# Kernel tuning notes

Measured on AMD Instinct MI355X. Metric: run time of the kernel, lower is better.

The kernel has to match this reference:

```python
import jax, jax.numpy as jnp
import numpy as np

B, S, C, H, D = 4, 1024, 1024, 16, 64
MAX_POS = 512
SPAN = min(max(S, S), MAX_POS)  # rel_attn_span = 512
SCALE = 1.0 / np.sqrt(3.0 * D)


def setup_inputs() -> dict:
    key = jax.random.key(0)
    ks = jax.random.split(key, 10)
    std = 0.02
    return {
        "hidden_states": jax.random.normal(ks[0], (B, S, C), jnp.float32),
        "rel_embeddings": jax.random.normal(ks[1], (2 * MAX_POS, C), jnp.float32),
        "Wq": jax.random.normal(ks[2], (C, H, D), jnp.float32) * std,
        "bq": jnp.zeros((H, D), jnp.float32),
        "Wk": jax.random.normal(ks[3], (C, H, D), jnp.float32) * std,
        "Wv": jax.random.normal(ks[4], (C, H, D), jnp.float32) * std,
        "bv": jnp.zeros((H, D), jnp.float32),
        "Wc2p": jax.random.normal(ks[5], (C, H, D), jnp.float32) * std,
        "Wp2c": jax.random.normal(ks[6], (C, H, D), jnp.float32) * std,
        "bp2c": jnp.zeros((H, D), jnp.float32),
        "Wo": jax.random.normal(ks[7], (C, C), jnp.float32) * std,
        "bo": jnp.zeros((C,), jnp.float32),
    }


def reference(hidden_states, rel_embeddings, Wq, bq, Wk, Wv, bv, Wc2p, Wp2c, bp2c, Wo, bo):
    # Projections: 'abc,cde->abde'  -> [B,S,H,D]
    q = jnp.einsum("bsc,chd->bshd", hidden_states, Wq) + bq
    k = jnp.einsum("bsc,chd->bshd", hidden_states, Wk)
    v = jnp.einsum("bsc,chd->bshd", hidden_states, Wv) + bv

    q = q * SCALE
    # content-to-content scores: 'aecd,abcd->acbe' -> [B,H,Q,K]
    scores = jnp.einsum("bkhd,bqhd->bhqk", k, q)

    # relative-position ids: rel_pos[q,k] = q - k, shape [S,S]
    ids = jnp.arange(S, dtype=jnp.int32)
    rel_pos = ids[:, None] - ids[None, :]

    # slice rel table to the active span (full table here since S >= MAX_POS)
    rel = rel_embeddings[MAX_POS - SPAN : MAX_POS + SPAN, :]  # [2*SPAN, C]

    # c2p: pos_key [2*SPAN,H,D]; scores [B,H,Q,2*SPAN]; gather along last axis
    pos_key = jnp.einsum("rc,chd->rhd", rel, Wc2p)
    c2p = jnp.einsum("bqhd,rhd->bhqr", q, pos_key)
    c2p_pos = jnp.clip(rel_pos + SPAN, 0, 2 * SPAN - 1)  # [Q,K]
    c2p_idx = jnp.broadcast_to(c2p_pos[None, None], (B, H, S, S))
    c2p_g = jnp.take_along_axis(c2p, c2p_idx, axis=-1)

    # p2c: pos_query (scaled) [2*SPAN,H,D]; scores [B,H,K,2*SPAN]
    pos_query = (jnp.einsum("rc,chd->rhd", rel, Wp2c) + bp2c) * SCALE
    p2c = jnp.einsum("bkhd,rhd->bhkr", k, pos_query)
    p2c_pos = jnp.clip(-rel_pos + SPAN, 0, 2 * SPAN - 1)  # [K,K]
    p2c_idx = jnp.broadcast_to(p2c_pos[None, None], (B, H, S, S))
    p2c_g = jnp.take_along_axis(p2c, p2c_idx, axis=-1)

    scores = scores + c2p_g + p2c_g
    # NOTE: source calls _masked_softmax without passing attention_mask -> plain softmax
    probs = jax.nn.softmax(scores, axis=-1)

    # 'acbe,aecd->abcd' -> [B,Q,H,D]
    attn_out = jnp.einsum("bhqk,bkhd->bqhd", probs, v)
    attn_out = attn_out.reshape(B, S, H * D)
    return jnp.einsum("bsc,cd->bsd", attn_out, Wo) + bo
```

## Files before the change

### kernel.cpp

```cpp
#include <hip/hip_runtime.h>
#include <cmath>

#define SCALE_F 0.07216878364870322f

typedef unsigned short u16;
typedef __attribute__((ext_vector_type(8))) __bf16 bf16x8;
typedef __attribute__((ext_vector_type(4))) float f32x4;
typedef __attribute__((ext_vector_type(16))) float f32x16;

#define MFMA16(a, b, c) __builtin_amdgcn_mfma_f32_16x16x32_bf16(a, b, c, 0, 0, 0)
#define MFMA32(a, b, c) __builtin_amdgcn_mfma_f32_32x32x16_bf16(a, b, c, 0, 0, 0)

__device__ __forceinline__ u16 f2bf(float x) {
    unsigned u = __float_as_uint(x);
    unsigned r = (u + 0x7fffu + ((u >> 16) & 1u)) >> 16;
    return (u16)r;
}
__device__ __forceinline__ float bf2f(u16 u) {
    return __uint_as_float(((unsigned)u) << 16);
}
__device__ __forceinline__ void split2(float x, u16& h, u16& l) {
    h = f2bf(x);
    l = f2bf(x - bf2f(h));
}

__device__ __forceinline__ void glds16(const u16* g, u16* s) {
    __builtin_amdgcn_global_load_lds(
        (const __attribute__((address_space(1))) unsigned int*)g,
        (__attribute__((address_space(3))) unsigned int*)s,
        16, 0, 0);
}

__device__ __forceinline__ bf16x8 frg(const u16* base, int row, int ch) {
    return *(const bf16x8*)(base + (row << 6) + ((ch ^ (row & 7)) << 3));
}

__global__ __launch_bounds__(256) void split_rows2(
    const float* __restrict__ x0, u16* __restrict__ h0, u16* __restrict__ l0,
    int nblk0,
    const float* __restrict__ x1, u16* __restrict__ h1, u16* __restrict__ l1)
{
    const float* x; u16* h; u16* l; int bx = blockIdx.x;
    if (bx < nblk0) { x = x0; h = h0; l = l0; }
    else { x = x1; h = h1; l = l1; bx -= nblk0; }
    int i = (bx * 256 + threadIdx.x) << 2;
    float4 v = *(const float4*)(x + i);
    ushort4 hv, lv;
    split2(v.x, hv.x, lv.x); split2(v.y, hv.y, lv.y);
    split2(v.z, hv.z, lv.z); split2(v.w, hv.w, lv.w);
    *(ushort4*)(h + i) = hv;
    *(ushort4*)(l + i) = lv;
}

__global__ __launch_bounds__(256) void transpose3(
    const float* __restrict__ W0, u16* __restrict__ Th0, u16* __restrict__ Tl0,
    const float* __restrict__ W1, u16* __restrict__ Th1, u16* __restrict__ Tl1,
    const float* __restrict__ W2, u16* __restrict__ Th2, u16* __restrict__ Tl2)
{
    const float* W; u16* Th; u16* Tl;
    if (blockIdx.z == 0)      { W = W0; Th = Th0; Tl = Tl0; }
    else if (blockIdx.z == 1) { W = W1; Th = Th1; Tl = Tl1; }
    else                      { W = W2; Th = Th2; Tl = Tl2; }
    __shared__ float t[64][65];
    const int tid = threadIdx.x;
    const int r = tid >> 4, c4 = (tid & 15) << 2;
    const int k0 = blockIdx.y << 6, n0 = blockIdx.x << 6;
#pragma unroll
    for (int p = 0; p < 4; ++p) {
        int row = (p << 4) + r;
        float4 v = *(const float4*)(W + (size_t)(k0 + row) * 1024 + n0 + c4);
        t[row][c4] = v.x; t[row][c4 + 1] = v.y; t[row][c4 + 2] = v.z; t[row][c4 + 3] = v.w;
    }
    __syncthreads();
#pragma unroll
    for (int p = 0; p < 4; ++p) {
        int nr = (p << 4) + r;
        float a = t[c4 + 0][nr];
        float b = t[c4 + 1][nr];
        float c = t[c4 + 2][nr];
        float d = t[c4 + 3][nr];
        ushort4 hv, lv;
        split2(a, hv.x, lv.x); split2(b, hv.y, lv.y);
        split2(c, hv.z, lv.z); split2(d, hv.w, lv.w);
        *(ushort4*)(Th + (size_t)(n0 + nr) * 1024 + k0 + c4) = hv;
        *(ushort4*)(Tl + (size_t)(n0 + nr) * 1024 + k0 + c4) = lv;
    }
}

struct GD {
    const u16 *Ah, *Al, *Bh, *Bl;
    const float* bias;
    float* Cf;
    u16 *Ch, *Cl;
    int N, K;
    float scale;
    int mode;
};

__global__ __launch_bounds__(256, 2) void gemm_mfma(GD d0, GD d1, int xsplit)
{
    __shared__ u16 sAh[128 * 32];
    __shared__ u16 sAl[128 * 32];
    __shared__ u16 sBh[128 * 32];
    __shared__ u16 sBl[128 * 32];

    const GD d = (blockIdx.x < (unsigned)xsplit) ? d0 : d1;
    const int bx = (blockIdx.x < (unsigned)xsplit) ? blockIdx.x : blockIdx.x - xsplit;
    const int N = d.N, K = d.K;

    const int tid = threadIdx.x;
    const int wv = tid >> 6, lane = tid & 63;
    const int quad = lane >> 4, ln = lane & 15;
    const int wr = wv & 1, wc = wv >> 1;
    const int m0 = blockIdx.y << 7, n0 = bx << 7;

    const u16* gsrc = (wv == 0) ? d.Ah : (wv == 1) ? d.Al : (wv == 2) ? d.Bh : d.Bl;
    u16* sdst = (wv == 0) ? sAh : (wv == 1) ? sAl : (wv == 2) ? sBh : sBl;
    const int row0 = (wv < 2) ? m0 : n0;
    const u16* gbase = gsrc + (size_t)(row0 + (lane >> 2)) * K + ((lane & 3) << 3);

    f32x4 acc[4][4];
#pragma unroll
    for (int f = 0; f < 4; ++f)
#pragma unroll
        for (int g = 0; g < 4; ++g) acc[f][g] = (f32x4){0.f, 0.f, 0.f, 0.f};

    const u16* pa_h = sAh + ((wr << 6) + ln) * 32 + (quad << 3);
    const u16* pa_l = sAl + ((wr << 6) + ln) * 32 + (quad << 3);
    const u16* pb_h = sBh + ((wc << 6) + ln) * 32 + (quad << 3);
    const u16* pb_l = sBl + ((wc << 6) + ln) * 32 + (quad << 3);

#pragma unroll
    for (int t = 0; t < 8; ++t)
        glds16(gbase + (size_t)(t << 4) * K, sdst + t * 512);

    for (int kt = 0; kt < K; kt += 32) {
        __syncthreads();
        bf16x8 bhv[4], blv[4], ahv[4], alv[4];
#pragma unroll
        for (int g = 0; g < 4; ++g) {
            bhv[g] = *(const bf16x8*)(pb_h + g * 512);
            blv[g] = *(const bf16x8*)(pb_l + g * 512);
            ahv[g] = *(const bf16x8*)(pa_h + g * 512);
            alv[g] = *(const bf16x8*)(pa_l + g * 512);
        }
        __syncthreads();
        if (kt + 32 < K) {
#pragma unroll
            for (int t = 0; t < 8; ++t)
                glds16(gbase + (size_t)(t << 4) * K + (kt + 32), sdst + t * 512);
        }
#pragma unroll
        for (int f = 0; f < 4; ++f) {
#pragma unroll
            for (int g = 0; g < 4; ++g) {
                acc[f][g] = MFMA16(ahv[f], bhv[g], acc[f][g]);
                acc[f][g] = MFMA16(ahv[f], blv[g], acc[f][g]);
                acc[f][g] = MFMA16(alv[f], bhv[g], acc[f][g]);
            }
        }
    }

    if (d.mode == 0) {
#pragma unroll
        for (int f = 0; f < 4; ++f) {
            int row = m0 + (wr << 6) + (f << 4) + (quad << 2);
#pragma unroll
            for (int g = 0; g < 4; ++g) {
                int col = n0 + (wc << 6) + (g << 4) + ln;
                float bb = d.bias ? d.bias[col] : 0.f;
#pragma unroll
                for (int r = 0; r < 4; ++r)
                    d.Cf[(size_t)(row + r) * N + col] = (acc[f][g][r] + bb) * d.scale;
            }
        }
    } else if (d.mode == 1) {
#pragma unroll
        for (int f = 0; f < 4; ++f) {
            int row = m0 + (wr << 6) + (f << 4) + (quad << 2);
#pragma unroll
            for (int g = 0; g < 4; ++g) {
                int col = n0 + (wc << 6) + (g << 4) + ln;
                float bb = d.bias ? d.bias[col] : 0.f;
#pragma unroll
                for (int r = 0; r < 4; ++r) {
                    float v = (acc[f][g][r] + bb) * d.scale;
                    u16 hh, ll;
                    split2(v, hh, ll);
                    d.Ch[(size_t)(row + r) * N + col] = hh;
                    d.Cl[(size_t)(row + r) * N + col] = ll;
                }
            }
        }
    } else if (d.mode == 2) {
#pragma unroll
        for (int f = 0; f < 4; ++f) {
            int row = m0 + (wr << 6) + (f << 4) + (quad << 2);
#pragma unroll
            for (int g = 0; g < 4; ++g) {
                int col = n0 + (wc << 6) + (g << 4) + ln;
                size_t obase = (size_t)(col >> 10) * 1048576 + (col & 1023);
#pragma unroll
                for (int r = 0; r < 4; ++r) {
                    float v = acc[f][g][r] + (d.bias ? d.bias[row + r] : 0.f);
                    u16 hh, ll;
                    split2(v, hh, ll);
                    size_t idx = obase + (size_t)(row + r) * 1024;
                    d.Ch[idx] = hh;
                    d.Cl[idx] = ll;
                }
            }
        }
    } else {
#pragma unroll
        for (int f = 0; f < 4; ++f) {
            int row = m0 + (wr << 6) + (f << 4) + (quad << 2);
#pragma unroll
            for (int g = 0; g < 4; ++g) {
                int col = n0 + (wc << 6) + (g << 4) + ln;
                float bb = d.bias ? d.bias[col] : 0.f;
#pragma unroll
                for (int r = 0; r < 4; ++r)
                    d.Ch[(size_t)(row + r) * N + col] =
                        f2bf((acc[f][g][r] + bb) * d.scale);
            }
        }
    }
}

__global__ __launch_bounds__(256, 2) void gemm_mfma_64(GD d0, GD d1, int xsplit)
{
    __shared__ u16 sAh[64 * 32];
    __shared__ u16 sAl[64 * 32];
    __shared__ u16 sBh[128 * 32];
    __shared__ u16 sBl[128 * 32];

    const GD d = (blockIdx.x < (unsigned)xsplit) ? d0 : d1;
    const int bx = (blockIdx.x < (unsigned)xsplit) ? blockIdx.x : blockIdx.x - xsplit;
    const int N = d.N, K = d.K;

    const int tid = threadIdx.x;
    const int wv = tid >> 6, lane = tid & 63;
    const int quad = lane >> 4, ln = lane & 15;
    const int wr = wv & 1, wc = wv >> 1;
    const int m0 = blockIdx.y << 6, n0 = bx << 7;

    const u16* gsrc = (wv == 0) ? d.Ah : (wv == 1) ? d.Al : (wv == 2) ? d.Bh : d.Bl;
    u16* sdst = (wv == 0) ? sAh : (wv == 1) ? sAl : (wv == 2) ? sBh : sBl;
    const int row0 = (wv < 2) ? m0 : n0;
    const int nt = (wv < 2) ? 4 : 8;
    const u16* gbase = gsrc + (size_t)(row0 + (lane >> 2)) * K + ((lane & 3) << 3);

    f32x4 acc[2][4];
#pragma unroll
    for (int f = 0; f < 2; ++f)
#pragma unroll
        for (int g = 0; g < 4; ++g) acc[f][g] = (f32x4){0.f, 0.f, 0.f, 0.f};

    const u16* pa_h = sAh + ((wr << 5) + ln) * 32 + (quad << 3);
    const u16* pa_l = sAl + ((wr << 5) + ln) * 32 + (quad << 3);
    const u16* pb_h = sBh + ((wc << 6) + ln) * 32 + (quad << 3);
    const u16* pb_l = sBl + ((wc << 6) + ln) * 32 + (quad << 3);

#pragma unroll
    for (int t = 0; t < 8; ++t)
        if (t < nt) glds16(gbase + (size_t)(t << 4) * K, sdst + t * 512);

    for (int kt = 0; kt < K; kt += 32) {
        __syncthreads();
        bf16x8 bhv[4], blv[4], ahv[2], alv[2];
#pragma unroll
        for (int g = 0; g < 4; ++g) {
            bhv[g] = *(const bf16x8*)(pb_h + g * 512);
            blv[g] = *(const bf16x8*)(pb_l + g * 512);
        }
#pragma unroll
        for (int f = 0; f < 2; ++f) {
            ahv[f] = *(const bf16x8*)(pa_h + f * 512);
            alv[f] = *(const bf16x8*)(pa_l + f * 512);
        }
        __syncthreads();
        if (kt + 32 < K) {
#pragma unroll
            for (int t = 0; t < 8; ++t)
                if (t < nt)
                    glds16(gbase + (size_t)(t << 4) * K + (kt + 32), sdst + t * 512);
        }
#pragma unroll
        for (int f = 0; f < 2; ++f) {
#pragma unroll
            for (int g = 0; g < 4; ++g) {
                acc[f][g] = MFMA16(ahv[f], bhv[g], acc[f][g]);
                acc[f][g] = MFMA16(ahv[f], blv[g], acc[f][g]);
                acc[f][g] = MFMA16(alv[f], bhv[g], acc[f][g]);
            }
        }
    }

    if (d.mode == 0) {
#pragma unroll
        for (int f = 0; f < 2; ++f) {
            int row = m0 + (wr << 5) + (f << 4) + (quad << 2);
#pragma unroll
            for (int g = 0; g < 4; ++g) {
                int col = n0 + (wc << 6) + (g << 4) + ln;
                float bb = d.bias ? d.bias[col] : 0.f;
#pragma unroll
                for (int r = 0; r < 4; ++r)
                    d.Cf[(size_t)(row + r) * N + col] = (acc[f][g][r] + bb) * d.scale;
            }
        }
    } else if (d.mode == 2) {
#pragma unroll
        for (int f = 0; f < 2; ++f) {
            int row = m0 + (wr << 5) + (f << 4) + (quad << 2);
#pragma unroll
            for (int g = 0; g < 4; ++g) {
                int col = n0 + (wc << 6) + (g << 4) + ln;
                size_t obase = (size_t)(col >> 10) * 1048576 + (col & 1023);
#pragma unroll
                for (int r = 0; r < 4; ++r) {
                    float v = acc[f][g][r] + (d.bias ? d.bias[row + r] : 0.f);
                    u16 hh, ll;
                    split2(v, hh, ll);
                    size_t idx = obase + (size_t)(row + r) * 1024;
                    d.Ch[idx] = hh;
                    d.Cl[idx] = ll;
                }
            }
        }
    } else if (d.mode == 3) {
#pragma unroll
        for (int f = 0; f < 2; ++f) {
            int row = m0 + (wr << 5) + (f << 4) + (quad << 2);
#pragma unroll
            for (int g = 0; g < 4; ++g) {
                int col = n0 + (wc << 6) + (g << 4) + ln;
                float bb = d.bias ? d.bias[col] : 0.f;
#pragma unroll
                for (int r = 0; r < 4; ++r)
                    d.Ch[(size_t)(row + r) * N + col] =
                        f2bf((acc[f][g][r] + bb) * d.scale);
            }
        }
    } else {
#pragma unroll
        for (int f = 0; f < 2; ++f) {
            int row = m0 + (wr << 5) + (f << 4) + (quad << 2);
#pragma unroll
            for (int g = 0; g < 4; ++g) {
                int col = n0 + (wc << 6) + (g << 4) + ln;
                float bb = d.bias ? d.bias[col] : 0.f;
#pragma unroll
                for (int r = 0; r < 4; ++r) {
                    float v = (acc[f][g][r] + bb) * d.scale;
                    u16 hh, ll;
                    split2(v, hh, ll);
                    d.Ch[(size_t)(row + r) * N + col] = hh;
                    d.Cl[(size_t)(row + r) * N + col] = ll;
                }
            }
        }
    }
}

__global__ __launch_bounds__(256, 2) void attn_mfma(
    const u16* Qh_g, const u16* Ql_g,
    const u16* __restrict__ Kh_g, const u16* __restrict__ Kl_g,
    const u16* __restrict__ VTh_g, const u16* __restrict__ VTl_g,
    const u16* __restrict__ PKh_g, const u16* __restrict__ PQh_g,
    u16* outh, u16* outl)
{
    __shared__ __align__(16) unsigned char smem[67840];
    u16* Kh_s  = (u16*)smem;
    u16* Kl_s  = (u16*)(smem + 8192);
    u16* PKs   = (u16*)(smem + 16384);
    u16* VTh_s = (u16*)(smem + 16384);
    u16* VTl_s = (u16*)(smem + 24576);
    u16* PQs   = (u16*)(smem + 32768);
    u16* Ph    = (u16*)(smem + 49152);
    u16* Pl    = (u16*)(smem + 58368);
    float* Mbase = (float*)(smem + 49152);
    float* l_s = (float*)(smem + 67584);

    const int tid = threadIdx.x;
    const int wv = tid >> 6, lane = tid & 63;
    const int half = lane >> 5, lc = lane & 31;
    const int rw = wv & 1, cw = wv >> 1;
    const int b = blockIdx.z, h = blockIdx.y;
    const int q0 = blockIdx.x << 6, hd0 = h << 6;
    float* Mw = Mbase + wv * 1056;

    const int rloc = lane >> 3;
    const int k4e  = (((lane & 7) ^ rloc) << 3);

    bf16x8 qfh[4], qfl[4], kfh[4], kfl[4];
    const size_t arow = ((size_t)(b * 1024 + q0 + (rw << 5) + lc) << 10) + hd0 + (half << 3);
    {
#pragma unroll
        for (int c = 0; c < 4; ++c) {
            qfh[c] = *(const bf16x8*)(Qh_g + arow + (c << 4));
            qfl[c] = *(const bf16x8*)(Ql_g + arow + (c << 4));
            kfh[c] = *(const bf16x8*)(Kh_g + arow + (c << 4));
            kfl[c] = *(const bf16x8*)(Kl_g + arow + (c << 4));
        }
    }
    if (tid < 64) l_s[tid] = 0.f;

    f32x16 o;
    float l_part[16];
#pragma unroll
    for (int r = 0; r < 16; ++r) { o[r] = 0.f; l_part[r] = 0.f; }

    const int sbC = (rw - cw + 1) << 5;
    const int sbP = (cw - rw + 1) << 5;

    {
#pragma unroll
        for (int t = 0; t < 2; ++t) {
            int call = wv + (t << 2);
            int row = (call << 3) + rloc;
            size_t g = ((size_t)(b * 1024 + 0 + row) << 10) + hd0 + k4e;
            glds16(Kh_g + g, Kh_s + (call << 9));
            glds16(Kl_g + g, Kl_s + (call << 9));
        }
        const int baseC = q0 + 449, baseP = -q0 + 449;
#pragma unroll
        for (int t = 0; t < 4; ++t) {
            int call = wv + (t << 2);
            int row = (call << 3) + rloc;
            int rc = min(max(baseC + row, 0), 1023);
            int rp = min(max(baseP + row, 0), 1023);
            glds16(PKh_g + (((size_t)rc << 10) + hd0 + k4e), PKs + (call << 9));
            glds16(PQh_g + (((size_t)rp << 10) + hd0 + k4e), PQs + (call << 9));
        }
    }
    __syncthreads();

    for (int kt = 0; kt < 16; ++kt) {
        const int k0 = kt << 6;
        f32x16 s;
#pragma unroll
        for (int r = 0; r < 16; ++r) s[r] = 0.f;
        {
            const int krow = (cw << 5) + lc;
#pragma unroll
            for (int c = 0; c < 4; ++c) {
                int ch = (c << 1) + half;
                bf16x8 bh = frg(Kh_s, krow, ch);
                bf16x8 bl = frg(Kl_s, krow, ch);
                s = MFMA32(qfh[c], bh, s);
                s = MFMA32(qfh[c], bl, s);
                s = MFMA32(qfl[c], bh, s);
            }
        }
        {
            f32x16 M0, M1;
#pragma unroll
            for (int r = 0; r < 16; ++r) { M0[r] = 0.f; M1[r] = 0.f; }
#pragma unroll
            for (int c = 0; c < 4; ++c) {
                int ch = (c << 1) + half;
                bf16x8 b0 = frg(PKs, sbC + lc, ch);
                bf16x8 b1 = frg(PKs, sbC + 32 + lc, ch);
                M0 = MFMA32(qfh[c], b0, M0); M0 = MFMA32(qfl[c], b0, M0);
                M1 = MFMA32(qfh[c], b1, M1); M1 = MFMA32(qfl[c], b1, M1);
            }
#pragma unroll
            for (int r = 0; r < 16; ++r) {
                int m = (r & 3) + ((r >> 2) << 3) + (half << 2);
                bool u = (lc >= m);
                float val = u ? M0[r] : M1[r];
                int nn = m - lc + (u ? 31 : -1);
                Mw[m * 33 + nn] = val;
            }
#pragma unroll
            for (int r = 0; r < 16; ++r) {
                int m = (r & 3) + ((r >> 2) << 3) + (half << 2);
                s[r] += Mw[m * 33 + lc];
            }
        }
        {
            f32x16 M0, M1;
#pragma unroll
            for (int r = 0; r < 16; ++r) { M0[r] = 0.f; M1[r] = 0.f; }
#pragma unroll
            for (int c = 0; c < 4; ++c) {
                int ch = (c << 1) + half;
                bf16x8 b0 = frg(PQs, sbP + lc, ch);
                bf16x8 b1 = frg(PQs, sbP + 32 + lc, ch);
                M0 = MFMA32(kfh[c], b0, M0); M0 = MFMA32(kfl[c], b0, M0);
                M1 = MFMA32(kfh[c], b1, M1); M1 = MFMA32(kfl[c], b1, M1);
            }
#pragma unroll
            for (int r = 0; r < 16; ++r) {
                int m = (r & 3) + ((r >> 2) << 3) + (half << 2);
                bool u = (lc >= 31 - m);
                float val = u ? M0[r] : M1[r];
                int nn = lc + m + (u ? -31 : 1);
                Mw[m * 33 + nn] = val;
            }
#pragma unroll
            for (int r = 0; r < 16; ++r) {
                int m = (r & 3) + ((r >> 2) << 3) + (half << 2);
                s[r] += Mw[m * 33 + lc];
            }
        }
#pragma unroll
        for (int r = 0; r < 16; ++r) {
            s[r] = __expf(s[r]);
            l_part[r] += s[r];
        }
        __syncthreads();
        {
#pragma unroll
            for (int t = 0; t < 2; ++t) {
                int call = wv + (t << 2);
                int row = (call << 3) + rloc;
                size_t g = ((size_t)((b * 16 + h) * 64 + row) << 10) + k0 + k4e;
                glds16(VTh_g + g, VTh_s + (call << 9));
                glds16(VTl_g + g, VTl_s + (call << 9));
            }
        }
#pragma unroll
        for (int r = 0; r < 16; ++r) {
            int m = (r & 3) + ((r >> 2) << 3) + (half << 2);
            int addr = ((rw << 5) + m) * 72 + (cw << 5) + lc;
            u16 hh, ll;
            split2(s[r], hh, ll);
            Ph[addr] = hh;
            Pl[addr] = ll;
        }
        __syncthreads();
        {
            const u16* ap  = Ph + ((rw << 5) + lc) * 72 + (half << 3);
            const u16* apl = Pl + ((rw << 5) + lc) * 72 + (half << 3);
            const int vrow = (cw << 5) + lc;
#pragma unroll
            for (int c = 0; c < 4; ++c) {
                int ch = (c << 1) + half;
                bf16x8 ah = *(const bf16x8*)(ap + (c << 4));
                bf16x8 al = *(const bf16x8*)(apl + (c << 4));
                bf16x8 bh = frg(VTh_s, vrow, ch);
                bf16x8 bl = frg(VTl_s, vrow, ch);
                o = MFMA32(ah, bh, o);
                o = MFMA32(ah, bl, o);
                o = MFMA32(al, bh, o);
            }
        }
        __syncthreads();
        {
            const int k0n = ((kt + 1) & 15) << 6;
#pragma unroll
            for (int t = 0; t < 2; ++t) {
                int call = wv + (t << 2);
                int row = (call << 3) + rloc;
                size_t g = ((size_t)(b * 1024 + k0n + row) << 10) + hd0 + k4e;
                glds16(Kh_g + g, Kh_s + (call << 9));
                glds16(Kl_g + g, Kl_s + (call << 9));
            }
            const int baseC = q0 - k0n + 449, baseP = k0n - q0 + 449;
#pragma unroll
            for (int t = 0; t < 4; ++t) {
                int call = wv + (t << 2);
                int row = (call << 3) + rloc;
                int rc = min(max(baseC + row, 0), 1023);
                int rp = min(max(baseP + row, 0), 1023);
                glds16(PKh_g + (((size_t)rc << 10) + hd0 + k4e), PKs + (call << 9));
                glds16(PQh_g + (((size_t)rp << 10) + hd0 + k4e), PQs + (call << 9));
            }
        }
        __syncthreads();
    }
#pragma unroll
    for (int r = 0; r < 16; ++r) {
        float v = l_part[r];
#pragma unroll
        for (int off = 1; off < 32; off <<= 1) v += __shfl_xor(v, off, 64);
        int m = (r & 3) + ((r >> 2) << 3) + (half << 2);
        if (lc == 0) atomicAdd(&l_s[(rw << 5) + m], v);
    }
    __syncthreads();
#pragma unroll
    for (int r = 0; r < 16; ++r) {
        int m = (r & 3) + ((r >> 2) << 3) + (half << 2);
        int row = (rw << 5) + m;
        float inv = 1.f / l_s[row];
        size_t g = ((size_t)(b * 1024 + q0 + row) << 10) + hd0 + (cw << 5) + lc;
        u16 hh, ll;
        split2(o[r] * inv, hh, ll);
        outh[g] = hh;
        outl[g] = ll;
    }
}

extern "C" void kernel_launch(void* const* d_in, const int* in_sizes, int n_in,
                              void* d_out, int out_size, void* d_ws, size_t ws_size,
                              hipStream_t stream)
{
    (void)in_sizes; (void)n_in; (void)out_size; (void)ws_size;
    const float* hidden = (const float*)d_in[0];
    const float* rel    = (const float*)d_in[1];
    const float* Wq   = (const float*)d_in[2];
    const float* bq   = (const float*)d_in[3];
    const float* Wk   = (const float*)d_in[4];
    const float* Wv   = (const float*)d_in[5];
    const float* bv   = (const float*)d_in[6];
    const float* Wc2p = (const float*)d_in[7];
    const float* Wp2c = (const float*)d_in[8];
    const float* bp2c = (const float*)d_in[9];
    const float* Wo   = (const float*)d_in[10];
    const float* bo   = (const float*)d_in[11];
    float* out = (float*)d_out;

    u16* U = (u16*)d_ws;
    const size_t MU = 1048576;
    u16* Hh  = U;              u16* Hl  = U + 4 * MU;
    u16* Rh  = U + 8 * MU;     u16* Rl  = U + 9 * MU;
    u16* WtAh = U + 10 * MU;   u16* WtAl = U + 11 * MU;
    u16* Qh  = U + 12 * MU;    u16* Ql  = U + 16 * MU;
    u16* Kh  = U + 20 * MU;    u16* Kl  = U + 24 * MU;
    u16* VTh = U + 28 * MU;    u16* VTl = U + 32 * MU;
    u16* WkTh = U + 28 * MU;   u16* WkTl = U + 29 * MU;
    u16* PKh = U + 0 * MU;
    u16* PQh = U + 2 * MU;
    u16* Wp2cTh = U + 4 * MU;  u16* Wp2cTl = U + 5 * MU;
    u16* WoTh = U + 6 * MU;    u16* WoTl = U + 7 * MU;

    dim3 blk(256);

    hipLaunchKernelGGL(split_rows2, dim3(5120), blk, 0, stream,
                       hidden, Hh, Hl, 4096, rel, Rh, Rl);

    hipLaunchKernelGGL(transpose3, dim3(16, 16, 2), blk, 0, stream,
                       Wq, WtAh, WtAl, Wk, WkTh, WkTl,
                       (const float*)nullptr, (u16*)nullptr, (u16*)nullptr);

    {
        GD dQ = {Hh, Hl, WtAh, WtAl, bq, nullptr, Qh, Ql, 1024, 1024, SCALE_F, 1};
        GD dK = {Hh, Hl, WkTh, WkTl, nullptr, nullptr, Kh, Kl, 1024, 1024, 1.f, 1};
        hipLaunchKernelGGL(gemm_mfma_64, dim3(16, 64), blk, 0, stream, dQ, dK, 8);
    }

    hipLaunchKernelGGL(transpose3, dim3(16, 16, 1), blk, 0, stream,
                       Wv, WtAh, WtAl,
                       (const float*)nullptr, (u16*)nullptr, (u16*)nullptr,
                       (const float*)nullptr, (u16*)nullptr, (u16*)nullptr);

    {
        GD dV = {WtAh, WtAl, Hh, Hl, bv, nullptr, VTh, VTl, 4096, 1024, 1.f, 2};
        hipLaunchKernelGGL(gemm_mfma_64, dim3(32, 16), blk, 0, stream, dV, dV, 9999);
    }

    hipLaunchKernelGGL(transpose3, dim3(16, 16, 3), blk, 0, stream,
                       Wc2p, WtAh, WtAl, Wp2c, Wp2cTh, Wp2cTl, Wo, WoTh, WoTl);

    {
        GD dPK = {Rh, Rl, WtAh, WtAl, nullptr, nullptr, PKh, nullptr, 1024, 1024, 1.f, 3};
        GD dPQ = {Rh, Rl, Wp2cTh, Wp2cTl, bp2c, nullptr, PQh, nullptr, 1024, 1024, SCALE_F, 3};
        hipLaunchKernelGGL(gemm_mfma_64, dim3(16, 16), blk, 0, stream, dPK, dPQ, 8);
    }

    hipLaunchKernelGGL(attn_mfma, dim3(16, 16, 4), blk, 0, stream,
                       Qh, Ql, Kh, Kl, VTh, VTl, PKh, PQh, Qh, Ql);

    {
        GD dO = {Qh, Ql, WoTh, WoTl, bo, out, nullptr, nullptr, 1024, 1024, 1.f, 0};
        hipLaunchKernelGGL(gemm_mfma_64, dim3(8, 64), blk, 0, stream, dO, dO, 9999);
    }
}
```

Measured before the change: 465.7 us.

## Fuse prep kernels and GEMM launches to cut kernel launch count

Merges the row-split and all weight-transpose kernels into one prep launch, fuses the Q/K/V projection GEMMs into one launch, and folds the Wo transpose into the PK/PQ GEMM launch. Scratch weight transposes are placed in the output buffer, which is overwritten later. This removes several launches and inter-kernel serialization gaps and lets independent work share the GPU. The cost is more branching per block and reliance on the output buffer being free scratch until the final GEMM.

```diff
diff --git a/kernel.cpp b/kernel.cpp
--- a/kernel.cpp
+++ b/kernel.cpp
@@ -35,36 +35,41 @@
     return *(const bf16x8*)(base + (row << 6) + ((ch ^ (row & 7)) << 3));
 }
 
-__global__ __launch_bounds__(256) void split_rows2(
+__global__ __launch_bounds__(256) void prep_fused(
     const float* __restrict__ x0, u16* __restrict__ h0, u16* __restrict__ l0,
-    int nblk0,
-    const float* __restrict__ x1, u16* __restrict__ h1, u16* __restrict__ l1)
-{
-    const float* x; u16* h; u16* l; int bx = blockIdx.x;
-    if (bx < nblk0) { x = x0; h = h0; l = l0; }
-    else { x = x1; h = h1; l = l1; bx -= nblk0; }
-    int i = (bx * 256 + threadIdx.x) << 2;
-    float4 v = *(const float4*)(x + i);
-    ushort4 hv, lv;
-    split2(v.x, hv.x, lv.x); split2(v.y, hv.y, lv.y);
-    split2(v.z, hv.z, lv.z); split2(v.w, hv.w, lv.w);
-    *(ushort4*)(h + i) = hv;
-    *(ushort4*)(l + i) = lv;
-}
-
-__global__ __launch_bounds__(256) void transpose3(
+    const float* __restrict__ x1, u16* __restrict__ h1, u16* __restrict__ l1,
     const float* __restrict__ W0, u16* __restrict__ Th0, u16* __restrict__ Tl0,
     const float* __restrict__ W1, u16* __restrict__ Th1, u16* __restrict__ Tl1,
-    const float* __restrict__ W2, u16* __restrict__ Th2, u16* __restrict__ Tl2)
+    const float* __restrict__ W2, u16* __restrict__ Th2, u16* __restrict__ Tl2,
+    const float* __restrict__ W3, u16* __restrict__ Th3, u16* __restrict__ Tl3,
+    const float* __restrict__ W4, u16* __restrict__ Th4, u16* __restrict__ Tl4)
 {
+    __shared__ float t[64][65];
+    int bx = blockIdx.x;
+    if (bx < 5120) {
+        const float* x; u16* h; u16* l;
+        if (bx < 4096) { x = x0; h = h0; l = l0; }
+        else { x = x1; h = h1; l = l1; bx -= 4096; }
+        int i = (bx * 256 + threadIdx.x) << 2;
+        float4 v = *(const float4*)(x + i);
+        ushort4 hv, lv;
+        split2(v.x, hv.x, lv.x); split2(v.y, hv.y, lv.y);
+        split2(v.z, hv.z, lv.z); split2(v.w, hv.w, lv.w);
+        *(ushort4*)(h + i) = hv;
+        *(ushort4*)(l + i) = lv;
+        return;
+    }
+    const int w = (bx - 5120) >> 8;
+    const int idx = (bx - 5120) & 255;
     const float* W; u16* Th; u16* Tl;
-    if (blockIdx.z == 0)      { W = W0; Th = Th0; Tl = Tl0; }
-    else if (blockIdx.z == 1) { W = W1; Th = Th1; Tl = Tl1; }
-    else                      { W = W2; Th = Th2; Tl = Tl2; }
-    __shared__ float t[64][65];
+    if (w == 0)      { W = W0; Th = Th0; Tl = Tl0; }
+    else if (w == 1) { W = W1; Th = Th1; Tl = Tl1; }
+    else if (w == 2) { W = W2; Th = Th2; Tl = Tl2; }
+    else if (w == 3) { W = W3; Th = Th3; Tl = Tl3; }
+    else             { W = W4; Th = Th4; Tl = Tl4; }
     const int tid = threadIdx.x;
     const int r = tid >> 4, c4 = (tid & 15) << 2;
-    const int k0 = blockIdx.y << 6, n0 = blockIdx.x << 6;
+    const int n0 = (idx & 15) << 6, k0 = (idx >> 4) << 6;
 #pragma unroll
     for (int p = 0; p < 4; ++p) {
         int row = (p << 4) + r;
@@ -97,61 +102,58 @@
     int mode;
 };
 
-__global__ __launch_bounds__(256, 2) void gemm_mfma(GD d0, GD d1, int xsplit)
+__device__ __forceinline__ void gemm64_body(
+    const GD& d, int m0, int n0, int tid,
+    u16* sAh, u16* sAl, u16* sBh, u16* sBl)
 {
-    __shared__ u16 sAh[128 * 32];
-    __shared__ u16 sAl[128 * 32];
-    __shared__ u16 sBh[128 * 32];
-    __shared__ u16 sBl[128 * 32];
-
-    const GD d = (blockIdx.x < (unsigned)xsplit) ? d0 : d1;
-    const int bx = (blockIdx.x < (unsigned)xsplit) ? blockIdx.x : blockIdx.x - xsplit;
     const int N = d.N, K = d.K;
-
-    const int tid = threadIdx.x;
     const int wv = tid >> 6, lane = tid & 63;
     const int quad = lane >> 4, ln = lane & 15;
     const int wr = wv & 1, wc = wv >> 1;
-    const int m0 = blockIdx.y << 7, n0 = bx << 7;
 
     const u16* gsrc = (wv == 0) ? d.Ah : (wv == 1) ? d.Al : (wv == 2) ? d.Bh : d.Bl;
     u16* sdst = (wv == 0) ? sAh : (wv == 1) ? sAl : (wv == 2) ? sBh : sBl;
     const int row0 = (wv < 2) ? m0 : n0;
+    const int nt = (wv < 2) ? 4 : 8;
     const u16* gbase = gsrc + (size_t)(row0 + (lane >> 2)) * K + ((lane & 3) << 3);
 
-    f32x4 acc[4][4];
-#pragma unroll
-    for (int f = 0; f < 4; ++f)
+    f32x4 acc[2][4];
+#pragma unroll
+    for (int f = 0; f < 2; ++f)
 #pragma unroll
         for (int g = 0; g < 4; ++g) acc[f][g] = (f32x4){0.f, 0.f, 0.f, 0.f};
 
-    const u16* pa_h = sAh + ((wr << 6) + ln) * 32 + (quad << 3);
-    const u16* pa_l = sAl + ((wr << 6) + ln) * 32 + (quad << 3);
+    const u16* pa_h = sAh + ((wr << 5) + ln) * 32 + (quad << 3);
+    const u16* pa_l = sAl + ((wr << 5) + ln) * 32 + (quad << 3);
     const u16* pb_h = sBh + ((wc << 6) + ln) * 32 + (quad << 3);
     const u16* pb_l = sBl + ((wc << 6) + ln) * 32 + (quad << 3);
 
 #pragma unroll
     for (int t = 0; t < 8; ++t)
-        glds16(gbase + (size_t)(t << 4) * K, sdst + t * 512);
+        if (t < nt) glds16(gbase + (size_t)(t << 4) * K, sdst + t * 512);
 
     for (int kt = 0; kt < K; kt += 32) {
         __syncthreads();
-        bf16x8 bhv[4], blv[4], ahv[4], alv[4];
+        bf16x8 bhv[4], blv[4], ahv[2], alv[2];
 #pragma unroll
         for (int g = 0; g < 4; ++g) {
             bhv[g] = *(const bf16x8*)(pb_h + g * 512);
             blv[g] = *(const bf16x8*)(pb_l + g * 512);
-            ahv[g] = *(const bf16x8*)(pa_h + g * 512);
-            alv[g] = *(const bf16x8*)(pa_l + g * 512);
+        }
+#pragma unroll
+        for (int f = 0; f < 2; ++f) {
+            ahv[f] = *(const bf16x8*)(pa_h + f * 512);
+            alv[f] = *(const bf16x8*)(pa_l + f * 512);
         }
         __syncthreads();
         if (kt + 32 < K) {
 #pragma unroll
             for (int t = 0; t < 8; ++t)
-                glds16(gbase + (size_t)(t << 4) * K + (kt + 32), sdst + t * 512);
-        }
-#pragma unroll
-        for (int f = 0; f < 4; ++f) {
+                if (t < nt)
+                    glds16(gbase + (size_t)(t << 4) * K + (kt + 32), sdst + t * 512);
+        }
+#pragma unroll
+        for (int f = 0; f < 2; ++f) {
 #pragma unroll
             for (int g = 0; g < 4; ++g) {
                 acc[f][g] = MFMA16(ahv[f], bhv[g], acc[f][g]);
@@ -163,8 +165,8 @@
 
     if (d.mode == 0) {
 #pragma unroll
-        for (int f = 0; f < 4; ++f) {
-            int row = m0 + (wr << 6) + (f << 4) + (quad << 2);
+        for (int f = 0; f < 2; ++f) {
+            int row = m0 + (wr << 5) + (f << 4) + (quad << 2);
 #pragma unroll
             for (int g = 0; g < 4; ++g) {
                 int col = n0 + (wc << 6) + (g << 4) + ln;
@@ -174,28 +176,10 @@
                     d.Cf[(size_t)(row + r) * N + col] = (acc[f][g][r] + bb) * d.scale;
             }
         }
-    } else if (d.mode == 1) {
-#pragma unroll
-        for (int f = 0; f < 4; ++f) {
-            int row = m0 + (wr << 6) + (f << 4) + (quad << 2);
-#pragma unroll
-            for (int g = 0; g < 4; ++g) {
-                int col = n0 + (wc << 6) + (g << 4) + ln;
-                float bb = d.bias ? d.bias[col] : 0.f;
-#pragma unroll
-                for (int r = 0; r < 4; ++r) {
-                    float v = (acc[f][g][r] + bb) * d.scale;
-                    u16 hh, ll;
-                    split2(v, hh, ll);
-                    d.Ch[(size_t)(row + r) * N + col] = hh;
-                    d.Cl[(size_t)(row + r) * N + col] = ll;
-                }
-            }
-        }
     } else if (d.mode == 2) {
 #pragma unroll
-        for (int f = 0; f < 4; ++f) {
-            int row = m0 + (wr << 6) + (f << 4) + (quad << 2);
+        for (int f = 0; f < 2; ++f) {
+            int row = m0 + (wr << 5) + (f << 4) + (quad << 2);
 #pragma unroll
             for (int g = 0; g < 4; ++g) {
                 int col = n0 + (wc << 6) + (g << 4) + ln;
@@ -211,124 +195,6 @@
                 }
             }
         }
-    } else {
-#pragma unroll
-        for (int f = 0; f < 4; ++f) {
-            int row = m0 + (wr << 6) + (f << 4) + (quad << 2);
-#pragma unroll
-            for (int g = 0; g < 4; ++g) {
-                int col = n0 + (wc << 6) + (g << 4) + ln;
-                float bb = d.bias ? d.bias[col] : 0.f;
-#pragma unroll
-                for (int r = 0; r < 4; ++r)
-                    d.Ch[(size_t)(row + r) * N + col] =
-                        f2bf((acc[f][g][r] + bb) * d.scale);
-            }
-        }
-    }
-}
-
-__global__ __launch_bounds__(256, 2) void gemm_mfma_64(GD d0, GD d1, int xsplit)
-{
-    __shared__ u16 sAh[64 * 32];
-    __shared__ u16 sAl[64 * 32];
-    __shared__ u16 sBh[128 * 32];
-    __shared__ u16 sBl[128 * 32];
-
-    const GD d = (blockIdx.x < (unsigned)xsplit) ? d0 : d1;
-    const int bx = (blockIdx.x < (unsigned)xsplit) ? blockIdx.x : blockIdx.x - xsplit;
-    const int N = d.N, K = d.K;
-
-    const int tid = threadIdx.x;
-    const int wv = tid >> 6, lane = tid & 63;
-    const int quad = lane >> 4, ln = lane & 15;
-    const int wr = wv & 1, wc = wv >> 1;
-    const int m0 = blockIdx.y << 6, n0 = bx << 7;
-
-    const u16* gsrc = (wv == 0) ? d.Ah : (wv == 1) ? d.Al : (wv == 2) ? d.Bh : d.Bl;
-    u16* sdst = (wv == 0) ? sAh : (wv == 1) ? sAl : (wv == 2) ? sBh : sBl;
-    const int row0 = (wv < 2) ? m0 : n0;
-    const int nt = (wv < 2) ? 4 : 8;
-    const u16* gbase = gsrc + (size_t)(row0 + (lane >> 2)) * K + ((lane & 3) << 3);
-
-    f32x4 acc[2][4];
-#pragma unroll
-    for (int f = 0; f < 2; ++f)
-#pragma unroll
-        for (int g = 0; g < 4; ++g) acc[f][g] = (f32x4){0.f, 0.f, 0.f, 0.f};
-
-    const u16* pa_h = sAh + ((wr << 5) + ln) * 32 + (quad << 3);
-    const u16* pa_l = sAl + ((wr << 5) + ln) * 32 + (quad << 3);
-    const u16* pb_h = sBh + ((wc << 6) + ln) * 32 + (quad << 3);
-    const u16* pb_l = sBl + ((wc << 6) + ln) * 32 + (quad << 3);
-
-#pragma unroll
-    for (int t = 0; t < 8; ++t)
-        if (t < nt) glds16(gbase + (size_t)(t << 4) * K, sdst + t * 512);
-
-    for (int kt = 0; kt < K; kt += 32) {
-        __syncthreads();
-        bf16x8 bhv[4], blv[4], ahv[2], alv[2];
-#pragma unroll
-        for (int g = 0; g < 4; ++g) {
-            bhv[g] = *(const bf16x8*)(pb_h + g * 512);
-            blv[g] = *(const bf16x8*)(pb_l + g * 512);
-        }
-#pragma unroll
-        for (int f = 0; f < 2; ++f) {
-            ahv[f] = *(const bf16x8*)(pa_h + f * 512);
-            alv[f] = *(const bf16x8*)(pa_l + f * 512);
-        }
-        __syncthreads();
-        if (kt + 32 < K) {
-#pragma unroll
-            for (int t = 0; t < 8; ++t)
-                if (t < nt)
-                    glds16(gbase + (size_t)(t << 4) * K + (kt + 32), sdst + t * 512);
-        }
-#pragma unroll
-        for (int f = 0; f < 2; ++f) {
-#pragma unroll
-            for (int g = 0; g < 4; ++g) {
-                acc[f][g] = MFMA16(ahv[f], bhv[g], acc[f][g]);
-                acc[f][g] = MFMA16(ahv[f], blv[g], acc[f][g]);
-                acc[f][g] = MFMA16(alv[f], bhv[g], acc[f][g]);
-            }
-        }
-    }
-
-    if (d.mode == 0) {
-#pragma unroll
-        for (int f = 0; f < 2; ++f) {
-            int row = m0 + (wr << 5) + (f << 4) + (quad << 2);
-#pragma unroll
-            for (int g = 0; g < 4; ++g) {
-                int col = n0 + (wc << 6) + (g << 4) + ln;
-                float bb = d.bias ? d.bias[col] : 0.f;
-#pragma unroll
-                for (int r = 0; r < 4; ++r)
-                    d.Cf[(size_t)(row + r) * N + col] = (acc[f][g][r] + bb) * d.scale;
-            }
-        }
-    } else if (d.mode == 2) {
-#pragma unroll
-        for (int f = 0; f < 2; ++f) {
-            int row = m0 + (wr << 5) + (f << 4) + (quad << 2);
-#pragma unroll
-            for (int g = 0; g < 4; ++g) {
-                int col = n0 + (wc << 6) + (g << 4) + ln;
-                size_t obase = (size_t)(col >> 10) * 1048576 + (col & 1023);
-#pragma unroll
-                for (int r = 0; r < 4; ++r) {
-                    float v = acc[f][g][r] + (d.bias ? d.bias[row + r] : 0.f);
-                    u16 hh, ll;
-                    split2(v, hh, ll);
-                    size_t idx = obase + (size_t)(row + r) * 1024;
-                    d.Ch[idx] = hh;
-                    d.Cl[idx] = ll;
-                }
-            }
-        }
     } else if (d.mode == 3) {
 #pragma unroll
         for (int f = 0; f < 2; ++f) {
@@ -360,6 +226,184 @@
                     d.Cl[(size_t)(row + r) * N + col] = ll;
                 }
             }
+        }
+    }
+}
+
+__global__ __launch_bounds__(256, 2) void gemm_mfma(GD d0, GD d1, int xsplit)
+{
+    __shared__ u16 sAh[128 * 32];
+    __shared__ u16 sAl[128 * 32];
+    __shared__ u16 sBh[128 * 32];
+    __shared__ u16 sBl[128 * 32];
+
+    const GD d = (blockIdx.x < (unsigned)xsplit) ? d0 : d1;
+    const int bx = (blockIdx.x < (unsigned)xsplit) ? blockIdx.x : blockIdx.x - xsplit;
+    const int N = d.N, K = d.K;
+
+    const int tid = threadIdx.x;
+    const int wv = tid >> 6, lane = tid & 63;
+    const int quad = lane >> 4, ln = lane & 15;
+    const int wr = wv & 1, wc = wv >> 1;
+    const int m0 = blockIdx.y << 7, n0 = bx << 7;
+
+    const u16* gsrc = (wv == 0) ? d.Ah : (wv == 1) ? d.Al : (wv == 2) ? d.Bh : d.Bl;
+    u16* sdst = (wv == 0) ? sAh : (wv == 1) ? sAl : (wv == 2) ? sBh : sBl;
+    const int row0 = (wv < 2) ? m0 : n0;
+    const u16* gbase = gsrc + (size_t)(row0 + (lane >> 2)) * K + ((lane & 3) << 3);
+
+    f32x4 acc[4][4];
+#pragma unroll
+    for (int f = 0; f < 4; ++f)
+#pragma unroll
+        for (int g = 0; g < 4; ++g) acc[f][g] = (f32x4){0.f, 0.f, 0.f, 0.f};
+
+    const u16* pa_h = sAh + ((wr << 6) + ln) * 32 + (quad << 3);
+    const u16* pa_l = sAl + ((wr << 6) + ln) * 32 + (quad << 3);
+    const u16* pb_h = sBh + ((wc << 6) + ln) * 32 + (quad << 3);
+    const u16* pb_l = sBl + ((wc << 6) + ln) * 32 + (quad << 3);
+
+#pragma unroll
+    for (int t = 0; t < 8; ++t)
+        glds16(gbase + (size_t)(t << 4) * K, sdst + t * 512);
+
+    for (int kt = 0; kt < K; kt += 32) {
+        __syncthreads();
+        bf16x8 bhv[4], blv[4], ahv[4], alv[4];
+#pragma unroll
+        for (int g = 0; g < 4; ++g) {
+            bhv[g] = *(const bf16x8*)(pb_h + g * 512);
+            blv[g] = *(const bf16x8*)(pb_l + g * 512);
+            ahv[g] = *(const bf16x8*)(pa_h + g * 512);
+            alv[g] = *(const bf16x8*)(pa_l + g * 512);
+        }
+        __syncthreads();
+        if (kt + 32 < K) {
+#pragma unroll
+            for (int t = 0; t < 8; ++t)
+                glds16(gbase + (size_t)(t << 4) * K + (kt + 32), sdst + t * 512);
+        }
+#pragma unroll
+        for (int f = 0; f < 4; ++f) {
+#pragma unroll
+            for (int g = 0; g < 4; ++g) {
+                acc[f][g] = MFMA16(ahv[f], bhv[g], acc[f][g]);
+                acc[f][g] = MFMA16(ahv[f], blv[g], acc[f][g]);
+                acc[f][g] = MFMA16(alv[f], bhv[g], acc[f][g]);
+            }
+        }
+    }
+
+    if (d.mode == 0) {
+#pragma unroll
+        for (int f = 0; f < 4; ++f) {
+            int row = m0 + (wr << 6) + (f << 4) + (quad << 2);
+#pragma unroll
+            for (int g = 0; g < 4; ++g) {
+                int col = n0 + (wc << 6) + (g << 4) + ln;
+                float bb = d.bias ? d.bias[col] : 0.f;
+#pragma unroll
+                for (int r = 0; r < 4; ++r)
+                    d.Cf[(size_t)(row + r) * N + col] = (acc[f][g][r] + bb) * d.scale;
+            }
+        }
+    } else {
+#pragma unroll
+        for (int f = 0; f < 4; ++f) {
+            int row = m0 + (wr << 6) + (f << 4) + (quad << 2);
+#pragma unroll
+            for (int g = 0; g < 4; ++g) {
+                int col = n0 + (wc << 6) + (g << 4) + ln;
+                float bb = d.bias ? d.bias[col] : 0.f;
+#pragma unroll
+                for (int r = 0; r < 4; ++r) {
+                    float v = (acc[f][g][r] + bb) * d.scale;
+                    u16 hh, ll;
+                    split2(v, hh, ll);
+                    d.Ch[(size_t)(row + r) * N + col] = hh;
+                    d.Cl[(size_t)(row + r) * N + col] = ll;
+                }
+            }
+        }
+    }
+}
+
+__global__ __launch_bounds__(256, 2) void gemm_mfma_64(GD d0, GD d1, int xsplit)
+{
+    __shared__ u16 sAh[64 * 32];
+    __shared__ u16 sAl[64 * 32];
+    __shared__ u16 sBh[128 * 32];
+    __shared__ u16 sBl[128 * 32];
+
+    const GD d = (blockIdx.x < (unsigned)xsplit) ? d0 : d1;
+    const int bx = (blockIdx.x < (unsigned)xsplit) ? blockIdx.x : blockIdx.x - xsplit;
+    gemm64_body(d, blockIdx.y << 6, bx << 7, threadIdx.x, sAh, sAl, sBh, sBl);
+}
+
+__global__ __launch_bounds__(256, 2) void gemm_fused3(GD dQ, GD dK, GD dV)
+{
+    __shared__ u16 sAh[64 * 32];
+    __shared__ u16 sAl[64 * 32];
+    __shared__ u16 sBh[128 * 32];
+    __shared__ u16 sBl[128 * 32];
+
+    const int lin = blockIdx.x;
+    GD d; int bx, by;
+    if (lin < 1024) {
+        const int bxp = lin & 15;
+        by = lin >> 4;
+        d = (bxp < 8) ? dQ : dK;
+        bx = bxp & 7;
+    } else {
+        const int lv = lin - 1024;
+        d = dV;
+        bx = lv & 31;
+        by = lv >> 5;
+    }
+    gemm64_body(d, by << 6, bx << 7, threadIdx.x, sAh, sAl, sBh, sBl);
+}
+
+__global__ __launch_bounds__(256, 2) void gemm_pkpq_wot(
+    GD d0, GD d1,
+    const float* __restrict__ W, u16* __restrict__ Th, u16* __restrict__ Tl)
+{
+    __shared__ __align__(16) unsigned char smem[24576];
+    const int bx = blockIdx.x;
+    if (bx < 256) {
+        u16* sAh = (u16*)smem;
+        u16* sAl = (u16*)(smem + 4096);
+        u16* sBh = (u16*)(smem + 8192);
+        u16* sBl = (u16*)(smem + 16384);
+        const int bxx = bx & 15;
+        const int by = bx >> 4;
+        const GD d = (bxx < 8) ? d0 : d1;
+        gemm64_body(d, by << 6, (bxx & 7) << 7, threadIdx.x, sAh, sAl, sBh, sBl);
+    } else {
+        float* t = (float*)smem;
+        const int idx = bx - 256;
+        const int n0 = (idx & 15) << 6, k0 = (idx >> 4) << 6;
+        const int tid = threadIdx.x;
+        const int r = tid >> 4, c4 = (tid & 15) << 2;
+#pragma unroll
+        for (int p = 0; p < 4; ++p) {
+            int row = (p << 4) + r;
+            float4 v = *(const float4*)(W + (size_t)(k0 + row) * 1024 + n0 + c4);
+            t[row * 65 + c4] = v.x; t[row * 65 + c4 + 1] = v.y;
+            t[row * 65 + c4 + 2] = v.z; t[row * 65 + c4 + 3] = v.w;
+        }
+        __syncthreads();
+#pragma unroll
+        for (int p = 0; p < 4; ++p) {
+            int nr = (p << 4) + r;
+            float a = t[(c4 + 0) * 65 + nr];
+            float b = t[(c4 + 1) * 65 + nr];
+            float c = t[(c4 + 2) * 65 + nr];
+            float d = t[(c4 + 3) * 65 + nr];
+            ushort4 hv, lv;
+            split2(a, hv.x, lv.x); split2(b, hv.y, lv.y);
+            split2(c, hv.z, lv.z); split2(d, hv.w, lv.w);
+            *(ushort4*)(Th + (size_t)(n0 + nr) * 1024 + k0 + c4) = hv;
+            *(ushort4*)(Tl + (size_t)(n0 + nr) * 1024 + k0 + c4) = lv;
         }
     }
 }
@@ -621,44 +665,38 @@
     u16* Qh  = U + 12 * MU;    u16* Ql  = U + 16 * MU;
     u16* Kh  = U + 20 * MU;    u16* Kl  = U + 24 * MU;
     u16* VTh = U + 28 * MU;    u16* VTl = U + 32 * MU;
-    u16* WkTh = U + 28 * MU;   u16* WkTl = U + 29 * MU;
     u16* PKh = U + 0 * MU;
     u16* PQh = U + 2 * MU;
-    u16* Wp2cTh = U + 4 * MU;  u16* Wp2cTl = U + 5 * MU;
     u16* WoTh = U + 6 * MU;    u16* WoTl = U + 7 * MU;
 
+    u16* OS = (u16*)out;
+    u16* WkTh = OS + 0 * MU;   u16* WkTl = OS + 1 * MU;
+    u16* WvTh = OS + 2 * MU;   u16* WvTl = OS + 3 * MU;
+    u16* Wc2pTh = OS + 4 * MU; u16* Wc2pTl = OS + 5 * MU;
+    u16* Wp2cTh = OS + 6 * MU; u16* Wp2cTl = OS + 7 * MU;
+
     dim3 blk(256);
 
-    hipLaunchKernelGGL(split_rows2, dim3(5120), blk, 0, stream,
-                       hidden, Hh, Hl, 4096, rel, Rh, Rl);
-
-    hipLaunchKernelGGL(transpose3, dim3(16, 16, 2), blk, 0, stream,
-                       Wq, WtAh, WtAl, Wk, WkTh, WkTl,
-                       (const float*)nullptr, (u16*)nullptr, (u16*)nullptr);
+    hipLaunchKernelGGL(prep_fused, dim3(6400), blk, 0, stream,
+                       hidden, Hh, Hl, rel, Rh, Rl,
+                       Wq, WtAh, WtAl,
+                       Wk, WkTh, WkTl,
+                       Wv, WvTh, WvTl,
+                       Wc2p, Wc2pTh, Wc2pTl,
+                       Wp2c, Wp2cTh, Wp2cTl);
 
     {
         GD dQ = {Hh, Hl, WtAh, WtAl, bq, nullptr, Qh, Ql, 1024, 1024, SCALE_F, 1};
         GD dK = {Hh, Hl, WkTh, WkTl, nullptr, nullptr, Kh, Kl, 1024, 1024, 1.f, 1};
-        hipLaunchKernelGGL(gemm_mfma_64, dim3(16, 64), blk, 0, stream, dQ, dK, 8);
-    }
-
-    hipLaunchKernelGGL(transpose3, dim3(16, 16, 1), blk, 0, stream,
-                       Wv, WtAh, WtAl,
-                       (const float*)nullptr, (u16*)nullptr, (u16*)nullptr,
-                       (const float*)nullptr, (u16*)nullptr, (u16*)nullptr);
+        GD dV = {WvTh, WvTl, Hh, Hl, bv, nullptr, VTh, VTl, 4096, 1024, 1.f, 2};
+        hipLaunchKernelGGL(gemm_fused3, dim3(1536), blk, 0, stream, dQ, dK, dV);
+    }
 
     {
-        GD dV = {WtAh, WtAl, Hh, Hl, bv, nullptr, VTh, VTl, 4096, 1024, 1.f, 2};
-        hipLaunchKernelGGL(gemm_mfma_64, dim3(32, 16), blk, 0, stream, dV, dV, 9999);
-    }
-
-    hipLaunchKernelGGL(transpose3, dim3(16, 16, 3), blk, 0, stream,
-                       Wc2p, WtAh, WtAl, Wp2c, Wp2cTh, Wp2cTl, Wo, WoTh, WoTl);
-
-    {
-        GD dPK = {Rh, Rl, WtAh, WtAl, nullptr, nullptr, PKh, nullptr, 1024, 1024, 1.f, 3};
+        GD dPK = {Rh, Rl, Wc2pTh, Wc2pTl, nullptr, nullptr, PKh, nullptr, 1024, 1024, 1.f, 3};
         GD dPQ = {Rh, Rl, Wp2cTh, Wp2cTl, bp2c, nullptr, PQh, nullptr, 1024, 1024, SCALE_F, 3};
-        hipLaunchKernelGGL(gemm_mfma_64, dim3(16, 16), blk, 0, stream, dPK, dPQ, 8);
+        hipLaunchKernelGGL(gemm_pkpq_wot, dim3(512), blk, 0, stream,
+                           dPK, dPQ, Wo, WoTh, WoTl);
     }
 
     hipLaunchKernelGGL(attn_mfma, dim3(16, 16, 4), blk, 0, stream,
```

New measurement: 453.6 us. 2.6% less time.
